# Performance work log

Hardware: AMD Instinct MI355X
Metric: run time of the kernel (lower is better)

## Reference

```python
import jax, jax.numpy as jnp
import numpy as np
from jax import lax

B, L, S, D = 2, 8, 512, 256


def setup_inputs() -> dict:
    key = jax.random.key(0)
    ks = jax.random.split(key, 12)
    s = 1.0 / np.sqrt(D)
    return {
        "features": jax.random.normal(ks[0], (B, L, S, D), jnp.float32),
        "source_features": jax.random.normal(ks[1], (B, S, D), jnp.float32),
        "target_features": jax.random.normal(ks[2], (B, S, D), jnp.float32),
        # GRU params (torch layout: [3D, D] with gate order r, z, n)
        "W_ih": jax.random.uniform(ks[3], (3 * D, D), jnp.float32, -s, s),
        "W_hh": jax.random.uniform(ks[4], (3 * D, D), jnp.float32, -s, s),
        "b_ih": jax.random.uniform(ks[5], (3 * D,), jnp.float32, -s, s),
        "b_hh": jax.random.uniform(ks[6], (3 * D,), jnp.float32, -s, s),
        # causal_predictor: Linear(2D, D) -> ReLU -> Linear(D, D) -> Sigmoid
        "W1": jax.random.uniform(ks[7], (D, 2 * D), jnp.float32, -s, s),
        "b1": jax.random.uniform(ks[8], (D,), jnp.float32, -s, s),
        "W2": jax.random.uniform(ks[9], (D, D), jnp.float32, -s, s),
        "b2": jax.random.uniform(ks[10], (D,), jnp.float32, -s, s),
    }


def _gru(x, W_ih, W_hh, b_ih, b_hh):
    # x: [N, T, D] batch-first; returns all hidden states [N, T, D]
    N, T, d = x.shape
    gx = jnp.einsum('ntd,gd->ntg', x, W_ih) + b_ih  # [N, T, 3D]

    def step(h, gx_t):
        gh = h @ W_hh.T + b_hh
        r = jax.nn.sigmoid(gx_t[:, :d] + gh[:, :d])
        z = jax.nn.sigmoid(gx_t[:, d:2 * d] + gh[:, d:2 * d])
        n = jnp.tanh(gx_t[:, 2 * d:] + r * gh[:, 2 * d:])
        h_new = (1.0 - z) * n + z * h
        return h_new, h_new

    h0 = jnp.zeros((N, d), x.dtype)
    _, outs = lax.scan(step, h0, jnp.swapaxes(gx, 0, 1))  # [T, N, D]
    return jnp.swapaxes(outs, 0, 1)


def reference(features, source_features, target_features,
              W_ih, W_hh, b_ih, b_hh, W1, b1, W2, b2):
    b, l, s, d = features.shape
    fdim = jnp.float32(d)

    # --- track_feature_evolution, vectorized over seq positions ---
    # per-position GRU over the layer axis == one GRU over a B*S batch
    x = jnp.transpose(features, (0, 2, 1, 3)).reshape(b * s, l, d)
    evolution_out = _gru(x, W_ih, W_hh, b_ih, b_hh).reshape(b, s, l, d)

    prev = features[:, :-1]            # [B, L-1, S, D]
    nxt = features[:, 1:]
    eps = jnp.float32(1e-8)
    na = jnp.maximum(jnp.linalg.norm(prev, axis=-1), eps)
    nb = jnp.maximum(jnp.linalg.norm(nxt, axis=-1), eps)
    stability = (jnp.sum(prev * nxt, axis=-1) / (na * nb)).mean(axis=0)  # [L-1, S]

    act = jnp.sum((features > 0.1).astype(jnp.float32), axis=-1)  # [B, L, S]
    emergence = (act[:, 1:] - act[:, :-1]).mean(axis=0) / fdim    # [L-1, S]
    decay = (act[:, :-1] - act[:, 1:]).mean(axis=0) / fdim        # [L-1, S]

    # --- compute_causal_strength ---
    # combined[b,s,i,:D] = source[b,s,:]; combined[b,s,i,D+k] = target[b,s,i] (all k)
    # first Linear(2D->D) therefore splits into:  source @ W1a^T  +  target_i * sum_k W1b[:,k]
    W1a = W1[:, :d]                     # [D, D]
    wb = jnp.sum(W1[:, d:], axis=1)     # [D]
    A = jnp.einsum('bsd,od->bso', source_features, W1a) + b1  # [B, S, D]
    h = A[:, :, None, :] + target_features[:, :, :, None] * wb  # [B, S, D(i), D(o)]
    h = jax.nn.relu(h)
    out2 = jax.nn.sigmoid(jnp.einsum('bsio,po->bsip', h, W2) + b2)  # [B, S, D, D]
    causal_matrix = out2.mean(axis=(0, 1))  # [D, D]

    return stability, emergence, decay, causal_matrix, evolution_out
```

## Files before the change

### kernel.cpp

```cpp
#include <hip/hip_runtime.h>
#include <hip/hip_bf16.h>
#include <stdint.h>

typedef unsigned short u16;
typedef __bf16 v8bf __attribute__((ext_vector_type(8)));
typedef float f32x4 __attribute__((ext_vector_type(4)));

#define WS_WB    0u
#define WS_WIHB  4096u
#define WS_WHHB  397312u
#define WS_W2B   790528u
#define WS_A     921600u
#define WS_GX    2097152u
#define WS_PART  27262976u
#define WS_FEATB 27262976u

#define OUT_STAB   0
#define OUT_EMER   3584
#define OUT_DECAY  7168
#define OUT_CAUSAL 10752
#define OUT_EVO    76288

__device__ __forceinline__ u16 f2bfu(float f){
    union { float f; uint32_t u; } v; v.f = f;
    uint32_t u = v.u;
    return (u16)((u + 0x7fffu + ((u >> 16) & 1u)) >> 16);
}
__device__ __forceinline__ float sigmoidf_fast(float x){
    float e = __builtin_amdgcn_exp2f(-1.4426950408889634f * x);
    return __builtin_amdgcn_rcpf(1.0f + e);
}
__device__ __forceinline__ float tanhf_fast(float x){
    float e = __builtin_amdgcn_exp2f(-2.8853900817779268f * x);
    return __builtin_amdgcn_rcpf(1.0f + e) * 2.0f - 1.0f;
}
__device__ __forceinline__ f32x4 mfma16(v8bf a, v8bf b, f32x4 c){
    return __builtin_amdgcn_mfma_f32_16x16x32_bf16(a, b, c, 0, 0, 0);
}
__device__ __forceinline__ v8bf cvt8(const float* p){
    float4 a = *(const float4*)p;
    float4 b = *(const float4*)(p + 4);
    v8bf r;
    r[0] = (__bf16)a.x; r[1] = (__bf16)a.y; r[2] = (__bf16)a.z; r[3] = (__bf16)a.w;
    r[4] = (__bf16)b.x; r[5] = (__bf16)b.y; r[6] = (__bf16)b.z; r[7] = (__bf16)b.w;
    return r;
}

__global__ __launch_bounds__(256) void k_pre(
        const float* __restrict__ feat, const float* __restrict__ src,
        const float* __restrict__ Wih,  const float* __restrict__ Whh,
        const float* __restrict__ W1,   const float* __restrict__ b1,
        const float* __restrict__ W2,
        u16* __restrict__ wihb, u16* __restrict__ whhb, u16* __restrict__ w2b,
        float* __restrict__ wb, u16* __restrict__ featb,
        float* __restrict__ A, float* __restrict__ out){
    const int bid = blockIdx.x, tid = threadIdx.x;
    if (bid < 64){
        const int bs0 = bid * 16;
        const int lane = tid & 63, w = tid >> 6;
        const int l15 = lane & 15, quad = lane >> 4;
        v8bf xa[8];
        for (int k = 0; k < 8; k++)
            xa[k] = cvt8(&src[(bs0 + l15) * 256 + k * 32 + quad * 8]);
        f32x4 acc[4];
        for (int nt = 0; nt < 4; nt++) acc[nt] = (f32x4){0.f, 0.f, 0.f, 0.f};
        for (int k = 0; k < 8; k++){
            int d0 = k * 32 + quad * 8;
            for (int nt = 0; nt < 4; nt++){
                int o = w * 64 + nt * 16 + l15;
                v8bf bfr = cvt8(&W1[o * 512 + d0]);
                acc[nt] = mfma16(xa[k], bfr, acc[nt]);
            }
        }
        for (int nt = 0; nt < 4; nt++){
            int o = w * 64 + nt * 16 + l15;
            float bb = b1[o];
            for (int r = 0; r < 4; r++)
                A[(bs0 + quad * 4 + r) * 256 + o] = acc[nt][r] + bb;
        }
    } else if (bid < 960){
        const int pair = (bid - 64) * 4 + (tid >> 6);
        const int l = pair >> 9, s = pair & 511;
        const int lane = tid & 63;
        float stab = 0.f, emer = 0.f;
        for (int b = 0; b < 2; b++){
            const float* p = feat + ((size_t)((b * 8 + l) * 512 + s)) * 256;
            const float* n = feat + ((size_t)((b * 8 + l + 1) * 512 + s)) * 256;
            float4 pv = *(const float4*)(p + lane * 4);
            float4 nv = *(const float4*)(n + lane * 4);
            float dot = pv.x * nv.x + pv.y * nv.y + pv.z * nv.z + pv.w * nv.w;
            float na2 = pv.x * pv.x + pv.y * pv.y + pv.z * pv.z + pv.w * pv.w;
            float nb2 = nv.x * nv.x + nv.y * nv.y + nv.z * nv.z + nv.w * nv.w;
            float ap = ((pv.x > 0.1f) ? 1.f : 0.f) + ((pv.y > 0.1f) ? 1.f : 0.f)
                     + ((pv.z > 0.1f) ? 1.f : 0.f) + ((pv.w > 0.1f) ? 1.f : 0.f);
            float an = ((nv.x > 0.1f) ? 1.f : 0.f) + ((nv.y > 0.1f) ? 1.f : 0.f)
                     + ((nv.z > 0.1f) ? 1.f : 0.f) + ((nv.w > 0.1f) ? 1.f : 0.f);
            for (int off = 32; off > 0; off >>= 1){
                dot += __shfl_xor(dot, off);
                na2 += __shfl_xor(na2, off);
                nb2 += __shfl_xor(nb2, off);
                ap  += __shfl_xor(ap,  off);
                an  += __shfl_xor(an,  off);
            }
            float na = fmaxf(__builtin_sqrtf(na2), 1e-8f);
            float nb = fmaxf(__builtin_sqrtf(nb2), 1e-8f);
            stab += dot / (na * nb);
            emer += (an - ap);
        }
        if (lane == 0){
            int o = l * 512 + s;
            float e = emer * 0.5f * (1.0f / 256.0f);
            out[OUT_STAB  + o] = stab * 0.5f;
            out[OUT_EMER  + o] = e;
            out[OUT_DECAY + o] = -e;
        }
    } else {
        int idx = (bid - 960) * 256 + tid;
        if (idx < 196608) {
            wihb[idx] = f2bfu(Wih[idx]);
        } else if (idx < 393216) {
            int i = idx - 196608; whhb[i] = f2bfu(Whh[i]);
        } else if (idx < 458752) {
            int i = idx - 393216; w2b[i] = f2bfu(W2[i]);
        } else if (idx < 459008) {
            int o = idx - 458752;
            float s = 0.f;
            const float4* p = (const float4*)&W1[o * 512 + 256];
            for (int j = 0; j < 64; j++){
                float4 v = p[j];
                s += v.x + v.y + v.z + v.w;
            }
            wb[o] = s;
        } else {
            int i = idx - 459008;
            featb[i] = f2bfu(feat[i]);
        }
    }
}

__global__ __launch_bounds__(256) void k_gx(
        const u16* __restrict__ featb, const u16* __restrict__ wihb,
        const float* __restrict__ bih, float* __restrict__ gxws){
    const int mb = blockIdx.x / 6, nb = blockIdx.x % 6;
    const int tid = threadIdx.x, lane = tid & 63, w = tid >> 6;
    const int l15 = lane & 15, quad = lane >> 4;

    __shared__ u16 blds[128 * 264];

    {
        int r = tid >> 1, half = tid & 1;
        const uint4* gsrc = (const uint4*)&wihb[(nb * 128 + r) * 256 + half * 128];
        uint4* ldst = (uint4*)&blds[r * 264 + half * 128];
        for (int j = 0; j < 16; j++) ldst[j] = gsrc[j];
    }

    v8bf af[2][8];
    for (int mt = 0; mt < 2; mt++){
        int r = mb * 128 + w * 32 + mt * 16 + l15;
        int n = r >> 3, t = r & 7;
        int b = n >> 9, s = n & 511;
        const u16* xp = featb + ((size_t)((b * 8 + t) * 512 + s)) * 256;
        for (int kk = 0; kk < 8; kk++)
            af[mt][kk] = *(const v8bf*)(xp + kk * 32 + quad * 8);
    }
    __syncthreads();

    f32x4 acc[2][8];
    for (int mt = 0; mt < 2; mt++) for (int nt = 0; nt < 8; nt++)
        acc[mt][nt] = (f32x4){0.f, 0.f, 0.f, 0.f};
    for (int kk = 0; kk < 8; kk++){
        int k0 = kk * 32 + quad * 8;
        for (int nt = 0; nt < 8; nt++){
            v8bf bf = *(const v8bf*)&blds[(nt * 16 + l15) * 264 + k0];
            acc[0][nt] = mfma16(af[0][kk], bf, acc[0][nt]);
            acc[1][nt] = mfma16(af[1][kk], bf, acc[1][nt]);
        }
    }
    for (int nt = 0; nt < 8; nt++){
        int g = nb * 128 + nt * 16 + l15;
        float bias = bih[g];
        for (int mt = 0; mt < 2; mt++)
            for (int rr = 0; rr < 4; rr++){
                int row = mb * 128 + w * 32 + mt * 16 + quad * 4 + rr;
                gxws[(size_t)row * 768 + g] = acc[mt][nt][rr] + bias;
            }
    }
}

__global__ __launch_bounds__(256, 2) void k_causal(
        const float* __restrict__ Aws, const float* __restrict__ wbws,
        const u16* __restrict__ w2b, const float* __restrict__ tgt,
        const float* __restrict__ b2, float* __restrict__ part){
    const int bid = blockIdx.x;
    const int chunk = bid >> 2, q = bid & 3;
    const int i0 = (q & 1) * 128, p0 = (q >> 1) * 128;
    const int tid = threadIdx.x, lane = tid & 63, w = tid >> 6;
    const int l15 = lane & 15, quad = lane >> 4;

    __shared__ u16  w2s[128 * 264];
    __shared__ float a_db[2][256];
    __shared__ float t_db[2][128];
    __shared__ float wb_s[256];

    {
        int r = tid >> 1, half = tid & 1;
        const uint4* gsrc = (const uint4*)&w2b[(p0 + r) * 256 + half * 128];
        uint4* ldst = (uint4*)&w2s[r * 264 + half * 128];
        for (int j = 0; j < 16; j++) ldst[j] = gsrc[j];
    }
    wb_s[tid] = wbws[tid];
    a_db[0][tid] = Aws[chunk * 8 * 256 + tid];
    if (tid < 128) t_db[0][tid] = tgt[(chunk * 8) * 256 + i0 + tid];

    float bb[8];
    for (int nt = 0; nt < 8; nt++) bb[nt] = b2[p0 + nt * 16 + l15];

    f32x4 sig[2][8];
    for (int mt = 0; mt < 2; mt++) for (int nt = 0; nt < 8; nt++)
        sig[mt][nt] = (f32x4){0.f, 0.f, 0.f, 0.f};

    for (int ss = 0; ss < 8; ss++){
        __syncthreads();
        if (ss < 7){
            int nb = (ss + 1) & 1;
            a_db[nb][tid] = Aws[(chunk * 8 + ss + 1) * 256 + tid];
            if (tid < 128) t_db[nb][tid] = tgt[(chunk * 8 + ss + 1) * 256 + i0 + tid];
        }
        const int cb = ss & 1;
        float tv0 = t_db[cb][w * 32 + l15];
        float tv1 = t_db[cb][w * 32 + 16 + l15];

        f32x4 acc[2][8];
        for (int mt = 0; mt < 2; mt++) for (int nt = 0; nt < 8; nt++)
            acc[mt][nt] = (f32x4){0.f, 0.f, 0.f, 0.f};

        for (int k = 0; k < 8; k++){
            const int o0 = k * 32 + quad * 8;
            float4 a0  = *(const float4*)&a_db[cb][o0];
            float4 a1  = *(const float4*)&a_db[cb][o0 + 4];
            float4 w0  = *(const float4*)&wb_s[o0];
            float4 w1v = *(const float4*)&wb_s[o0 + 4];
            v8bf afr0, afr1;
            {
                float t = tv0;
                afr0[0] = (__bf16)fmaxf(fmaf(t, w0.x,  a0.x), 0.f);
                afr0[1] = (__bf16)fmaxf(fmaf(t, w0.y,  a0.y), 0.f);
                afr0[2] = (__bf16)fmaxf(fmaf(t, w0.z,  a0.z), 0.f);
                afr0[3] = (__bf16)fmaxf(fmaf(t, w0.w,  a0.w), 0.f);
                afr0[4] = (__bf16)fmaxf(fmaf(t, w1v.x, a1.x), 0.f);
                afr0[5] = (__bf16)fmaxf(fmaf(t, w1v.y, a1.y), 0.f);
                afr0[6] = (__bf16)fmaxf(fmaf(t, w1v.z, a1.z), 0.f);
                afr0[7] = (__bf16)fmaxf(fmaf(t, w1v.w, a1.w), 0.f);
            }
            {
                float t = tv1;
                afr1[0] = (__bf16)fmaxf(fmaf(t, w0.x,  a0.x), 0.f);
                afr1[1] = (__bf16)fmaxf(fmaf(t, w0.y,  a0.y), 0.f);
                afr1[2] = (__bf16)fmaxf(fmaf(t, w0.z,  a0.z), 0.f);
                afr1[3] = (__bf16)fmaxf(fmaf(t, w0.w,  a0.w), 0.f);
                afr1[4] = (__bf16)fmaxf(fmaf(t, w1v.x, a1.x), 0.f);
                afr1[5] = (__bf16)fmaxf(fmaf(t, w1v.y, a1.y), 0.f);
                afr1[6] = (__bf16)fmaxf(fmaf(t, w1v.z, a1.z), 0.f);
                afr1[7] = (__bf16)fmaxf(fmaf(t, w1v.w, a1.w), 0.f);
            }
            for (int nt = 0; nt < 8; nt++){
                v8bf bfr = *(const v8bf*)&w2s[(nt * 16 + l15) * 264 + o0];
                acc[0][nt] = mfma16(afr0, bfr, acc[0][nt]);
                acc[1][nt] = mfma16(afr1, bfr, acc[1][nt]);
            }
        }
        for (int mt = 0; mt < 2; mt++)
            for (int nt = 0; nt < 8; nt++)
                for (int r = 0; r < 4; r++)
                    sig[mt][nt][r] += sigmoidf_fast(acc[mt][nt][r] + bb[nt]);
    }

    float* pp = part + (size_t)chunk * 65536;
    for (int mt = 0; mt < 2; mt++)
        for (int r = 0; r < 4; r++){
            int i = i0 + w * 32 + mt * 16 + quad * 4 + r;
            for (int nt = 0; nt < 8; nt++){
                int p = p0 + nt * 16 + l15;
                pp[i * 256 + p] = sig[mt][nt][r];
            }
        }
}

__global__ __launch_bounds__(512) void k_final(
        const float* __restrict__ gxws, const u16* __restrict__ whhb,
        const float* __restrict__ bhh, const float* __restrict__ part,
        float* __restrict__ out){
    if (blockIdx.x >= 64){
        const int idx = (blockIdx.x - 64) * 512 + threadIdx.x;
        float s = 0.f;
        for (int c = 0; c < 128; c++)
            s += part[(size_t)c * 65536 + idx];
        out[OUT_CAUSAL + idx] = s * (1.0f / 1024.0f);
        return;
    }
    const int n0 = blockIdx.x * 16;
    const int tid = threadIdx.x, lane = tid & 63, wv = tid >> 6;
    const int l15 = lane & 15, quad = lane >> 4;
    const int g0 = wv * 96;

    __shared__ float h_lds[16 * 260];
    __shared__ float g_lds[16 * 776];

    v8bf wreg[3][8];
    for (int nt = 0; nt < 3; nt++)
        for (int k = 0; k < 8; k++)
            wreg[nt][k] = *(const v8bf*)&whhb[(g0 + nt * 16 + l15) * 256 + k * 32 + quad * 8];

    float bias[6];
    for (int nt = 0; nt < 6; nt++) bias[nt] = bhh[g0 + nt * 16 + l15];

    for (int e = tid; e < 16 * 260; e += 512) h_lds[e] = 0.f;

    const int seq = tid >> 5, d0 = (tid & 31) * 8;
    const float* gxbase = gxws + (size_t)(n0 + seq) * 8 * 768 + d0;
    float* evobase = out + OUT_EVO + (size_t)(n0 + seq) * 8 * 256 + d0;
    __syncthreads();

    for (int t = 0; t < 8; t++){
        v8bf ha[8];
        for (int k = 0; k < 8; k++)
            ha[k] = cvt8(&h_lds[l15 * 260 + k * 32 + quad * 8]);
        f32x4 acc[6];
        for (int nt = 0; nt < 6; nt++) acc[nt] = (f32x4){0.f, 0.f, 0.f, 0.f};
        for (int k = 0; k < 8; k++){
            int dk = k * 32 + quad * 8;
            acc[0] = mfma16(ha[k], wreg[0][k], acc[0]);
            acc[1] = mfma16(ha[k], wreg[1][k], acc[1]);
            acc[2] = mfma16(ha[k], wreg[2][k], acc[2]);
            for (int nt = 3; nt < 6; nt++){
                v8bf bf = *(const v8bf*)&whhb[(g0 + nt * 16 + l15) * 256 + dk];
                acc[nt] = mfma16(ha[k], bf, acc[nt]);
            }
        }
        for (int nt = 0; nt < 6; nt++){
            int g = g0 + nt * 16 + l15;
            for (int rr = 0; rr < 4; rr++)
                g_lds[(quad * 4 + rr) * 776 + g] = acc[nt][rr] + bias[nt];
        }
        const float* gxp = gxbase + (size_t)t * 768;
        float4 x0a = *(const float4*)(gxp);
        float4 x0b = *(const float4*)(gxp + 4);
        float4 x1a = *(const float4*)(gxp + 256);
        float4 x1b = *(const float4*)(gxp + 260);
        float4 x2a = *(const float4*)(gxp + 512);
        float4 x2b = *(const float4*)(gxp + 516);
        __syncthreads();
        {
            const float* gh = &g_lds[seq * 776];
            float* hp = &h_lds[seq * 260 + d0];
            float4 g0a = *(const float4*)&gh[d0];
            float4 g0b = *(const float4*)&gh[d0 + 4];
            float4 g1a = *(const float4*)&gh[256 + d0];
            float4 g1b = *(const float4*)&gh[260 + d0];
            float4 g2a = *(const float4*)&gh[512 + d0];
            float4 g2b = *(const float4*)&gh[516 + d0];
            float4 h0 = *(const float4*)hp;
            float4 h1 = *(const float4*)(hp + 4);
            float gxr[8] = {x0a.x, x0a.y, x0a.z, x0a.w, x0b.x, x0b.y, x0b.z, x0b.w};
            float gxz[8] = {x1a.x, x1a.y, x1a.z, x1a.w, x1b.x, x1b.y, x1b.z, x1b.w};
            float gxn[8] = {x2a.x, x2a.y, x2a.z, x2a.w, x2b.x, x2b.y, x2b.z, x2b.w};
            float ghr[8] = {g0a.x, g0a.y, g0a.z, g0a.w, g0b.x, g0b.y, g0b.z, g0b.w};
            float ghz[8] = {g1a.x, g1a.y, g1a.z, g1a.w, g1b.x, g1b.y, g1b.z, g1b.w};
            float ghn[8] = {g2a.x, g2a.y, g2a.z, g2a.w, g2b.x, g2b.y, g2b.z, g2b.w};
            float hold[8] = {h0.x, h0.y, h0.z, h0.w, h1.x, h1.y, h1.z, h1.w};
            float hn[8];
            #pragma unroll
            for (int j = 0; j < 8; j++){
                float r  = sigmoidf_fast(gxr[j] + ghr[j]);
                float z  = sigmoidf_fast(gxz[j] + ghz[j]);
                float nn = tanhf_fast(fmaf(r, ghn[j], gxn[j]));
                hn[j] = (1.f - z) * nn + z * hold[j];
            }
            float4 v0 = {hn[0], hn[1], hn[2], hn[3]};
            float4 v1 = {hn[4], hn[5], hn[6], hn[7]};
            *(float4*)hp       = v0;
            *(float4*)(hp + 4) = v1;
            float* ep = evobase + (size_t)t * 256;
            *(float4*)ep       = v0;
            *(float4*)(ep + 4) = v1;
        }
        __syncthreads();
    }
}

extern "C" void kernel_launch(void* const* d_in, const int* in_sizes, int n_in,
                              void* d_out, int out_size, void* d_ws, size_t ws_size,
                              hipStream_t stream){
    const float* feat = (const float*)d_in[0];
    const float* src  = (const float*)d_in[1];
    const float* tgt  = (const float*)d_in[2];
    const float* Wih  = (const float*)d_in[3];
    const float* Whh  = (const float*)d_in[4];
    const float* bih  = (const float*)d_in[5];
    const float* bhh  = (const float*)d_in[6];
    const float* W1   = (const float*)d_in[7];
    const float* b1   = (const float*)d_in[8];
    const float* W2   = (const float*)d_in[9];
    const float* b2   = (const float*)d_in[10];
    float* out = (float*)d_out;
    char* ws = (char*)d_ws;

    float* wb   = (float*)(ws + WS_WB);
    u16*   wihb = (u16*)(ws + WS_WIHB);
    u16*   whhb = (u16*)(ws + WS_WHHB);
    u16*   w2b  = (u16*)(ws + WS_W2B);
    float* Aws  = (float*)(ws + WS_A);
    float* gxws = (float*)(ws + WS_GX);
    float* part = (float*)(ws + WS_PART);
    u16*   featb= (u16*)(ws + WS_FEATB);

    k_pre   <<<10945, 256, 0, stream>>>(feat, src, Wih, Whh, W1, b1, W2,
                                        wihb, whhb, w2b, wb, featb, Aws, out);
    k_gx    <<<384,   256, 0, stream>>>(featb, wihb, bih, gxws);
    k_causal<<<512,   256, 0, stream>>>(Aws, wb, w2b, tgt, b2, part);
    k_final <<<192,   512, 0, stream>>>(gxws, whhb, bhh, part, out);
}
```

Measured before the change: 227.1 us.

## Merge gx and causal kernels, drop bf16 feature copy, vectorize weight conversion

The separate bf16 copy of the features is removed, so the gx GEMM now reads fp32 features and converts them in registers. The gx and causal kernels are merged into a single launch whose blocks branch by index and share one raw shared-memory buffer, which removes a launch boundary and lets the two independent workloads overlap. Weight conversion in the pre-kernel packs 8 values per thread with vector stores, cutting the pre-kernel grid size considerably. In exchange, gx blocks read twice as many feature bytes, and the merged kernel's shared-memory footprint may limit occupancy.

```diff
diff --git a/kernel.cpp b/kernel.cpp
--- a/kernel.cpp
+++ b/kernel.cpp
@@ -13,7 +13,6 @@
 #define WS_A     921600u
 #define WS_GX    2097152u
 #define WS_PART  27262976u
-#define WS_FEATB 27262976u
 
 #define OUT_STAB   0
 #define OUT_EMER   3584
@@ -52,8 +51,7 @@
         const float* __restrict__ W1,   const float* __restrict__ b1,
         const float* __restrict__ W2,
         u16* __restrict__ wihb, u16* __restrict__ whhb, u16* __restrict__ w2b,
-        float* __restrict__ wb, u16* __restrict__ featb,
-        float* __restrict__ A, float* __restrict__ out){
+        float* __restrict__ wb, float* __restrict__ A, float* __restrict__ out){
     const int bid = blockIdx.x, tid = threadIdx.x;
     if (bid < 64){
         const int bs0 = bid * 16;
@@ -115,15 +113,23 @@
             out[OUT_DECAY + o] = -e;
         }
     } else {
-        int idx = (bid - 960) * 256 + tid;
-        if (idx < 196608) {
-            wihb[idx] = f2bfu(Wih[idx]);
-        } else if (idx < 393216) {
-            int i = idx - 196608; whhb[i] = f2bfu(Whh[i]);
-        } else if (idx < 458752) {
-            int i = idx - 393216; w2b[i] = f2bfu(W2[i]);
-        } else if (idx < 459008) {
-            int o = idx - 458752;
+        int idx8 = (bid - 960) * 256 + tid;
+        if (idx8 < 57344){
+            const float* srcp;
+            u16* dstp;
+            if (idx8 < 24576){ srcp = Wih + idx8 * 8;             dstp = wihb + idx8 * 8; }
+            else if (idx8 < 49152){ int i = idx8 - 24576; srcp = Whh + i * 8; dstp = whhb + i * 8; }
+            else { int i = idx8 - 49152; srcp = W2 + i * 8; dstp = w2b + i * 8; }
+            float4 a = *(const float4*)srcp;
+            float4 b = *(const float4*)(srcp + 4);
+            union { u16 h[8]; uint4 v; } pk;
+            pk.h[0] = f2bfu(a.x); pk.h[1] = f2bfu(a.y);
+            pk.h[2] = f2bfu(a.z); pk.h[3] = f2bfu(a.w);
+            pk.h[4] = f2bfu(b.x); pk.h[5] = f2bfu(b.y);
+            pk.h[6] = f2bfu(b.z); pk.h[7] = f2bfu(b.w);
+            *(uint4*)dstp = pk.v;
+        } else if (idx8 < 57600){
+            int o = idx8 - 57344;
             float s = 0.f;
             const float4* p = (const float4*)&W1[o * 512 + 256];
             for (int j = 0; j < 64; j++){
@@ -131,76 +137,73 @@
                 s += v.x + v.y + v.z + v.w;
             }
             wb[o] = s;
-        } else {
-            int i = idx - 459008;
-            featb[i] = f2bfu(feat[i]);
-        }
-    }
-}
-
-__global__ __launch_bounds__(256) void k_gx(
-        const u16* __restrict__ featb, const u16* __restrict__ wihb,
-        const float* __restrict__ bih, float* __restrict__ gxws){
-    const int mb = blockIdx.x / 6, nb = blockIdx.x % 6;
+        }
+    }
+}
+
+__global__ __launch_bounds__(256, 2) void k_mid(
+        const float* __restrict__ feat, const u16* __restrict__ wihb,
+        const float* __restrict__ bih,  float* __restrict__ gxws,
+        const float* __restrict__ Aws,  const float* __restrict__ wbws,
+        const u16* __restrict__ w2b,    const float* __restrict__ tgt,
+        const float* __restrict__ b2,   float* __restrict__ part){
+    __shared__ __align__(16) unsigned char smem[71680];
     const int tid = threadIdx.x, lane = tid & 63, w = tid >> 6;
     const int l15 = lane & 15, quad = lane >> 4;
 
-    __shared__ u16 blds[128 * 264];
-
-    {
-        int r = tid >> 1, half = tid & 1;
-        const uint4* gsrc = (const uint4*)&wihb[(nb * 128 + r) * 256 + half * 128];
-        uint4* ldst = (uint4*)&blds[r * 264 + half * 128];
-        for (int j = 0; j < 16; j++) ldst[j] = gsrc[j];
-    }
-
-    v8bf af[2][8];
-    for (int mt = 0; mt < 2; mt++){
-        int r = mb * 128 + w * 32 + mt * 16 + l15;
-        int n = r >> 3, t = r & 7;
-        int b = n >> 9, s = n & 511;
-        const u16* xp = featb + ((size_t)((b * 8 + t) * 512 + s)) * 256;
-        for (int kk = 0; kk < 8; kk++)
-            af[mt][kk] = *(const v8bf*)(xp + kk * 32 + quad * 8);
-    }
-    __syncthreads();
-
-    f32x4 acc[2][8];
-    for (int mt = 0; mt < 2; mt++) for (int nt = 0; nt < 8; nt++)
-        acc[mt][nt] = (f32x4){0.f, 0.f, 0.f, 0.f};
-    for (int kk = 0; kk < 8; kk++){
-        int k0 = kk * 32 + quad * 8;
+    if (blockIdx.x < 384){
+        const int mb = blockIdx.x / 6, nb = blockIdx.x % 6;
+        u16* blds = (u16*)smem;
+
+        {
+            int r = tid >> 1, half = tid & 1;
+            const uint4* gsrc = (const uint4*)&wihb[(nb * 128 + r) * 256 + half * 128];
+            uint4* ldst = (uint4*)&blds[r * 264 + half * 128];
+            for (int j = 0; j < 16; j++) ldst[j] = gsrc[j];
+        }
+
+        v8bf af[2][8];
+        for (int mt = 0; mt < 2; mt++){
+            int r = mb * 128 + w * 32 + mt * 16 + l15;
+            int n = r >> 3, t = r & 7;
+            int b = n >> 9, s = n & 511;
+            const float* xp = feat + ((size_t)((b * 8 + t) * 512 + s)) * 256;
+            for (int kk = 0; kk < 8; kk++)
+                af[mt][kk] = cvt8(xp + kk * 32 + quad * 8);
+        }
+        __syncthreads();
+
+        f32x4 acc[2][8];
+        for (int mt = 0; mt < 2; mt++) for (int nt = 0; nt < 8; nt++)
+            acc[mt][nt] = (f32x4){0.f, 0.f, 0.f, 0.f};
+        for (int kk = 0; kk < 8; kk++){
+            int k0 = kk * 32 + quad * 8;
+            for (int nt = 0; nt < 8; nt++){
+                v8bf bf = *(const v8bf*)&blds[(nt * 16 + l15) * 264 + k0];
+                acc[0][nt] = mfma16(af[0][kk], bf, acc[0][nt]);
+                acc[1][nt] = mfma16(af[1][kk], bf, acc[1][nt]);
+            }
+        }
         for (int nt = 0; nt < 8; nt++){
-            v8bf bf = *(const v8bf*)&blds[(nt * 16 + l15) * 264 + k0];
-            acc[0][nt] = mfma16(af[0][kk], bf, acc[0][nt]);
-            acc[1][nt] = mfma16(af[1][kk], bf, acc[1][nt]);
-        }
-    }
-    for (int nt = 0; nt < 8; nt++){
-        int g = nb * 128 + nt * 16 + l15;
-        float bias = bih[g];
-        for (int mt = 0; mt < 2; mt++)
-            for (int rr = 0; rr < 4; rr++){
-                int row = mb * 128 + w * 32 + mt * 16 + quad * 4 + rr;
-                gxws[(size_t)row * 768 + g] = acc[mt][nt][rr] + bias;
-            }
-    }
-}
-
-__global__ __launch_bounds__(256, 2) void k_causal(
-        const float* __restrict__ Aws, const float* __restrict__ wbws,
-        const u16* __restrict__ w2b, const float* __restrict__ tgt,
-        const float* __restrict__ b2, float* __restrict__ part){
-    const int bid = blockIdx.x;
-    const int chunk = bid >> 2, q = bid & 3;
+            int g = nb * 128 + nt * 16 + l15;
+            float bias = bih[g];
+            for (int mt = 0; mt < 2; mt++)
+                for (int rr = 0; rr < 4; rr++){
+                    int row = mb * 128 + w * 32 + mt * 16 + quad * 4 + rr;
+                    gxws[(size_t)row * 768 + g] = acc[mt][nt][rr] + bias;
+                }
+        }
+        return;
+    }
+
+    const int bidc = blockIdx.x - 384;
+    const int chunk = bidc >> 2, q = bidc & 3;
     const int i0 = (q & 1) * 128, p0 = (q >> 1) * 128;
-    const int tid = threadIdx.x, lane = tid & 63, w = tid >> 6;
-    const int l15 = lane & 15, quad = lane >> 4;
-
-    __shared__ u16  w2s[128 * 264];
-    __shared__ float a_db[2][256];
-    __shared__ float t_db[2][128];
-    __shared__ float wb_s[256];
+
+    u16*  w2s  = (u16*)smem;
+    float* a_db = (float*)(smem + 67584);
+    float* t_db = (float*)(smem + 69632);
+    float* wb_s = (float*)(smem + 70656);
 
     {
         int r = tid >> 1, half = tid & 1;
@@ -209,8 +212,8 @@
         for (int j = 0; j < 16; j++) ldst[j] = gsrc[j];
     }
     wb_s[tid] = wbws[tid];
-    a_db[0][tid] = Aws[chunk * 8 * 256 + tid];
-    if (tid < 128) t_db[0][tid] = tgt[(chunk * 8) * 256 + i0 + tid];
+    a_db[tid] = Aws[chunk * 8 * 256 + tid];
+    if (tid < 128) t_db[tid] = tgt[(chunk * 8) * 256 + i0 + tid];
 
     float bb[8];
     for (int nt = 0; nt < 8; nt++) bb[nt] = b2[p0 + nt * 16 + l15];
@@ -223,12 +226,12 @@
         __syncthreads();
         if (ss < 7){
             int nb = (ss + 1) & 1;
-            a_db[nb][tid] = Aws[(chunk * 8 + ss + 1) * 256 + tid];
-            if (tid < 128) t_db[nb][tid] = tgt[(chunk * 8 + ss + 1) * 256 + i0 + tid];
+            a_db[nb * 256 + tid] = Aws[(chunk * 8 + ss + 1) * 256 + tid];
+            if (tid < 128) t_db[nb * 128 + tid] = tgt[(chunk * 8 + ss + 1) * 256 + i0 + tid];
         }
         const int cb = ss & 1;
-        float tv0 = t_db[cb][w * 32 + l15];
-        float tv1 = t_db[cb][w * 32 + 16 + l15];
+        float tv0 = t_db[cb * 128 + w * 32 + l15];
+        float tv1 = t_db[cb * 128 + w * 32 + 16 + l15];
 
         f32x4 acc[2][8];
         for (int mt = 0; mt < 2; mt++) for (int nt = 0; nt < 8; nt++)
@@ -236,8 +239,8 @@
 
         for (int k = 0; k < 8; k++){
             const int o0 = k * 32 + quad * 8;
-            float4 a0  = *(const float4*)&a_db[cb][o0];
-            float4 a1  = *(const float4*)&a_db[cb][o0 + 4];
+            float4 a0  = *(const float4*)&a_db[cb * 256 + o0];
+            float4 a1  = *(const float4*)&a_db[cb * 256 + o0 + 4];
             float4 w0  = *(const float4*)&wb_s[o0];
             float4 w1v = *(const float4*)&wb_s[o0 + 4];
             v8bf afr0, afr1;
@@ -412,11 +415,10 @@
     float* Aws  = (float*)(ws + WS_A);
     float* gxws = (float*)(ws + WS_GX);
     float* part = (float*)(ws + WS_PART);
-    u16*   featb= (u16*)(ws + WS_FEATB);
-
-    k_pre   <<<10945, 256, 0, stream>>>(feat, src, Wih, Whh, W1, b1, W2,
-                                        wihb, whhb, w2b, wb, featb, Aws, out);
-    k_gx    <<<384,   256, 0, stream>>>(featb, wihb, bih, gxws);
-    k_causal<<<512,   256, 0, stream>>>(Aws, wb, w2b, tgt, b2, part);
-    k_final <<<192,   512, 0, stream>>>(gxws, whhb, bhh, part, out);
-}
+
+    k_pre  <<<1185, 256, 0, stream>>>(feat, src, Wih, Whh, W1, b1, W2,
+                                      wihb, whhb, w2b, wb, Aws, out);
+    k_mid  <<<896,  256, 0, stream>>>(feat, wihb, bih, gxws,
+                                      Aws, wb, w2b, tgt, b2, part);
+    k_final<<<192,  512, 0, stream>>>(gxws, whhb, bhh, part, out);
+}
```

New measurement: 222.5 us. -2.0%, faster.
